# Kernel tuning notes

Hardware: AMD Instinct MI355X
Metric: run time of the kernel (lower is better)

Reference implementation:

```python
import jax, jax.numpy as jnp
import numpy as np

B, N, E, D = 1, 50000, 800000, 128


def _mlp(x, w1, b1, w2, b2, w3, b3):
    # MLP(in, hidden, out, l=2): Linear+ReLU, Linear+ReLU, Linear
    h = jax.nn.relu(x @ w1 + b1)
    h = jax.nn.relu(h @ w2 + b2)
    return h @ w3 + b3


def _glorot(key, shape):
    fan_in, fan_out = shape[0], shape[1]
    lim = np.sqrt(6.0 / (fan_in + fan_out)).astype(np.float32)
    return jax.random.uniform(key, shape, jnp.float32, -lim, lim)


def setup_inputs() -> dict:
    key = jax.random.key(0)
    ks = jax.random.split(key, 16)
    inp = {
        "nodes": jax.random.normal(ks[0], (B, N, D), jnp.float32),
        "senders": jax.random.randint(ks[1], (E,), 0, N, jnp.int32),
        "receivers": jax.random.randint(ks[2], (E,), 0, N, jnp.int32),
        # message MLP params: 2D -> D -> D -> D
        "mw1": _glorot(ks[3], (2 * D, D)), "mb1": jnp.zeros((D,), jnp.float32),
        "mw2": _glorot(ks[4], (D, D)),     "mb2": jnp.zeros((D,), jnp.float32),
        "mw3": _glorot(ks[5], (D, D)),     "mb3": jnp.zeros((D,), jnp.float32),
        # node MLP params: 2D -> D -> D -> D
        "nw1": _glorot(ks[6], (2 * D, D)), "nb1": jnp.zeros((D,), jnp.float32),
        "nw2": _glorot(ks[7], (D, D)),     "nb2": jnp.zeros((D,), jnp.float32),
        "nw3": _glorot(ks[8], (D, D)),     "nb3": jnp.zeros((D,), jnp.float32),
    }
    return inp


def reference(nodes, senders, receivers,
              mw1, mb1, mw2, mb2, mw3, mb3,
              nw1, nb1, nw2, nb2, nw3, nb3):
    # gather endpoint features: [B, E, 2D]
    edge_in = jnp.concatenate((nodes[:, receivers], nodes[:, senders]), axis=-1)
    messages = _mlp(edge_in, mw1, mb1, mw2, mb2, mw3, mb3)  # [B, E, D]
    # scatter-add messages into receiver inbox: [B, N, D]
    inbox = jnp.zeros_like(nodes).at[:, receivers].add(messages)
    node_in = jnp.concatenate((nodes, inbox), axis=-1)  # [B, N, 2D]
    return nodes + _mlp(node_in, nw1, nb1, nw2, nb2, nw3, nb3)
```

## Files before the change

### kernel.cpp

```cpp
#include <hip/hip_runtime.h>
#include <hip/hip_bf16.h>
#include <stdint.h>

typedef __bf16 bf16;
typedef bf16 bf16x8 __attribute__((ext_vector_type(8)));
typedef float f32x4 __attribute__((ext_vector_type(4)));

#define N_NODES 50000
#define FEAT 128
#define NB_SCAN ((N_NODES + 1023) / 1024)

static constexpr size_t UV_BYTES    = (size_t)N_NODES * 256 * 2;
static constexpr size_t INBOX_BYTES = (size_t)N_NODES * FEAT * 4;

#define WUV_OFF 0
#define WM2_OFF 32768
#define WM3_OFF 49152
#define WN1_OFF 65536
#define WN2_OFF 98304
#define WN3_OFF 114688
#define W_TOTAL 131072
static constexpr size_t W_BYTES = (size_t)W_TOTAL * 2;

__device__ __forceinline__ bf16x8 cvt_f32x8_bf16(const float* __restrict__ p) {
  float4 f0 = *(const float4*)p;
  float4 f1 = *(const float4*)(p + 4);
  bf16x8 t;
  t[0] = (bf16)f0.x; t[1] = (bf16)f0.y; t[2] = (bf16)f0.z; t[3] = (bf16)f0.w;
  t[4] = (bf16)f1.x; t[5] = (bf16)f1.y; t[6] = (bf16)f1.z; t[7] = (bf16)f1.w;
  return t;
}

__global__ void prep_weights_kernel(const float* __restrict__ mw1, const float* __restrict__ mw2,
                                    const float* __restrict__ mw3, const float* __restrict__ nw1,
                                    const float* __restrict__ nw2, const float* __restrict__ nw3,
                                    bf16* __restrict__ w) {
  int i = blockIdx.x * blockDim.x + threadIdx.x;
  if (i >= W_TOTAL) return;
  float v;
  if (i < WM2_OFF) {
    int c = i >> 7, k = i & 127;
    v = (c < 128) ? mw1[k * 128 + c] : mw1[(128 + k) * 128 + (c - 128)];
  } else if (i < WM3_OFF) {
    int j = i - WM2_OFF; int c = j >> 7, k = j & 127;
    v = mw2[k * 128 + c];
  } else if (i < WN1_OFF) {
    int j = i - WM3_OFF; int c = j >> 7, k = j & 127;
    v = mw3[k * 128 + c];
  } else if (i < WN2_OFF) {
    int j = i - WN1_OFF; int c = j >> 8, k = j & 255;
    v = nw1[k * 128 + c];
  } else if (i < WN3_OFF) {
    int j = i - WN2_OFF; int c = j >> 7, k = j & 127;
    v = nw2[k * 128 + c];
  } else {
    int j = i - WN3_OFF; int c = j >> 7, k = j & 127;
    v = nw3[k * 128 + c];
  }
  w[i] = (bf16)v;
}

__global__ void hist_kernel(const int* __restrict__ receivers, int* __restrict__ cnt, int E) {
  int i = blockIdx.x * blockDim.x + threadIdx.x;
  if (i < E) atomicAdd(&cnt[receivers[i]], 1);
}

__global__ __launch_bounds__(1024) void scan1_kernel(const int* __restrict__ cnt,
                                                     int* __restrict__ offs,
                                                     int* __restrict__ bsum) {
  __shared__ int s[1024];
  const int tid = threadIdx.x;
  const int g = blockIdx.x * 1024 + tid;
  int x = (g < N_NODES) ? cnt[g] : 0;
  s[tid] = x;
  __syncthreads();
  for (int off = 1; off < 1024; off <<= 1) {
    int v = (tid >= off) ? s[tid - off] : 0;
    __syncthreads();
    s[tid] += v;
    __syncthreads();
  }
  if (g < N_NODES) offs[g] = s[tid] - x;
  if (tid == 1023) bsum[blockIdx.x] = s[tid];
}

__global__ void scan2_kernel(int* __restrict__ bsum) {
  __shared__ int s[64];
  const int tid = threadIdx.x;
  int x = (tid < NB_SCAN) ? bsum[tid] : 0;
  s[tid] = x;
  __syncthreads();
  for (int off = 1; off < 64; off <<= 1) {
    int v = (tid >= off) ? s[tid - off] : 0;
    __syncthreads();
    s[tid] += v;
    __syncthreads();
  }
  if (tid < NB_SCAN) bsum[tid] = s[tid] - x;
}

__global__ void scatter_ids_kernel(const int* __restrict__ senders,
                                   const int* __restrict__ receivers,
                                   const int* __restrict__ offs, const int* __restrict__ bsum,
                                   int* __restrict__ cur,
                                   int* __restrict__ sSend, int* __restrict__ sRecv, int E) {
  int i = blockIdx.x * blockDim.x + threadIdx.x;
  if (i < E) {
    int r = receivers[i];
    int slot = offs[r] + bsum[r >> 10] + atomicAdd(&cur[r], 1);
    sSend[slot] = senders[i];
    sRecv[slot] = r;
  }
}

__global__ void inbox_init_kernel(const int* __restrict__ cnt, const float* __restrict__ mb3,
                                  float* __restrict__ inbox) {
  int i = blockIdx.x * blockDim.x + threadIdx.x;
  if (i >= N_NODES * 32) return;
  int n = i >> 5, q = i & 31;
  float c = (float)cnt[n];
  float4 b = *(const float4*)(mb3 + q * 4);
  float4 o = {c * b.x, c * b.y, c * b.z, c * b.w};
  *(float4*)(inbox + (size_t)n * FEAT + q * 4) = o;
}

__global__ __launch_bounds__(512) void uv_gemm_kernel(const float* __restrict__ nodes,
                                                      const bf16* __restrict__ wuvt,
                                                      const float* __restrict__ mb1,
                                                      bf16* __restrict__ uv) {
  const int tid = threadIdx.x;
  const int lane = tid & 63, wid = tid >> 6;
  const int wm = wid >> 2, wn = wid & 3;
  const int rBase = blockIdx.x * 128 + wm * 64;
  const int cBase = wn * 64;
  const int l15 = lane & 15, ka = (lane >> 4) * 8, rj = (lane >> 4) * 4;

  f32x4 acc[4][4];
#pragma unroll
  for (int mi = 0; mi < 4; ++mi)
#pragma unroll
    for (int ni = 0; ni < 4; ++ni) acc[mi][ni] = (f32x4){0.f, 0.f, 0.f, 0.f};

#pragma unroll
  for (int kk = 0; kk < 4; ++kk) {
    const int k0 = kk * 32 + ka;
    bf16x8 a[4], b[4];
#pragma unroll
    for (int mi = 0; mi < 4; ++mi) {
      int r = rBase + mi * 16 + l15;
      if (r > N_NODES - 1) r = N_NODES - 1;
      a[mi] = cvt_f32x8_bf16(nodes + (size_t)r * FEAT + k0);
    }
#pragma unroll
    for (int ni = 0; ni < 4; ++ni) {
      int c = cBase + ni * 16 + l15;
      b[ni] = *(const bf16x8*)(wuvt + (size_t)c * 128 + k0);
    }
#pragma unroll
    for (int mi = 0; mi < 4; ++mi)
#pragma unroll
      for (int ni = 0; ni < 4; ++ni)
        acc[mi][ni] = __builtin_amdgcn_mfma_f32_16x16x32_bf16(a[mi], b[ni], acc[mi][ni], 0, 0, 0);
  }
#pragma unroll
  for (int mi = 0; mi < 4; ++mi)
#pragma unroll
    for (int ni = 0; ni < 4; ++ni) {
      int c = cBase + ni * 16 + l15;
      float bias = (c < FEAT) ? mb1[c] : 0.f;
#pragma unroll
      for (int j = 0; j < 4; ++j) {
        int r = rBase + mi * 16 + rj + j;
        if (r < N_NODES) uv[(size_t)r * 256 + c] = (bf16)(acc[mi][ni][j] + bias);
      }
    }
}

__device__ __forceinline__ void seg_reduce(const f32x4 (&acc3)[2][8], int idr,
                                           int lane, int l15, int rj,
                                           float* __restrict__ inbox) {
  int nxt = __shfl(idr, (lane & 31) + 1);
  bool bnd = ((lane & 31) == 31) || (idr != nxt);
  unsigned long long bm = __ballot(bnd);
  uint32_t mask = (uint32_t)(bm & 0xffffffffull);
  int lo = 0;
  while (mask) {
    int hi = __ffs(mask) - 1;
    mask &= mask - 1;
    int recv = __shfl(idr, hi);
    if (recv >= 0) {
      float s[8];
#pragma unroll
      for (int ni = 0; ni < 8; ++ni) {
        float x = 0.f;
#pragma unroll
        for (int mi = 0; mi < 2; ++mi)
#pragma unroll
          for (int j = 0; j < 4; ++j) {
            int row = mi * 16 + rj + j;
            x += (row >= lo && row <= hi) ? acc3[mi][ni][j] : 0.f;
          }
        x += __shfl_xor(x, 16);
        x += __shfl_xor(x, 32);
        s[ni] = x;
      }
      if (lane < 16) {
        float* dst = inbox + (size_t)recv * FEAT + l15;
#pragma unroll
        for (int ni = 0; ni < 8; ++ni) unsafeAtomicAdd(dst + ni * 16, s[ni]);
      }
    }
    lo = hi + 1;
  }
}

__global__ __launch_bounds__(256, 3) void edge_kernel(const bf16* __restrict__ uv,
                                                      const int* __restrict__ sSend,
                                                      const int* __restrict__ sRecv,
                                                      const bf16* __restrict__ wm2t,
                                                      const bf16* __restrict__ wm3t,
                                                      const float* __restrict__ mb2,
                                                      float* __restrict__ inbox, int E) {
  __shared__ bf16 hbuf[4][32 * 128];
  const int tid = threadIdx.x, lane = tid & 63, wid = tid >> 6;
  const int l15 = lane & 15, ka = (lane >> 4) * 8, rj = (lane >> 4) * 4;
  const int l31 = lane & 31;
  bf16* hw = hbuf[wid];

  const int e0 = (blockIdx.x * 4 + wid) * 32;
  if (e0 >= E) return;

  int e = e0 + l31;
  bool val = e < E;
  int ec = val ? e : E - 1;
  int idr = val ? sRecv[ec] : -1;
  int ids = sSend[ec];

  int rid[2], sid[2];
#pragma unroll
  for (int mi = 0; mi < 2; ++mi) {
    int row = mi * 16 + l15;
    int rv = __shfl(idr, row);
    rid[mi] = rv < 0 ? 0 : rv;
    sid[mi] = __shfl(ids, row);
  }
  bf16x8 afr[2][4];
#pragma unroll
  for (int mi = 0; mi < 2; ++mi) {
    const bf16* up = uv + (size_t)rid[mi] * 256;
    const bf16* vp = uv + (size_t)sid[mi] * 256 + 128;
#pragma unroll
    for (int kk = 0; kk < 4; ++kk) {
      bf16x8 u8 = *(const bf16x8*)(up + kk * 32 + ka);
      bf16x8 v8 = *(const bf16x8*)(vp + kk * 32 + ka);
      bf16x8 h;
#pragma unroll
      for (int x = 0; x < 8; ++x) {
        float s = (float)u8[x] + (float)v8[x];
        h[x] = (bf16)(s > 0.f ? s : 0.f);
      }
      afr[mi][kk] = h;
    }
  }

  f32x4 acc[2][8];
#pragma unroll
  for (int mi = 0; mi < 2; ++mi)
#pragma unroll
    for (int ni = 0; ni < 8; ++ni) acc[mi][ni] = (f32x4){0.f, 0.f, 0.f, 0.f};
  __builtin_amdgcn_s_setprio(1);
#pragma unroll
  for (int kk = 0; kk < 4; ++kk) {
    const int k0 = kk * 32 + ka;
    bf16x8 b[8];
#pragma unroll
    for (int ni = 0; ni < 8; ++ni) {
      int c = ni * 16 + l15;
      b[ni] = *(const bf16x8*)(wm2t + (size_t)c * 128 + k0);
    }
#pragma unroll
    for (int mi = 0; mi < 2; ++mi)
#pragma unroll
      for (int ni = 0; ni < 8; ++ni)
        acc[mi][ni] = __builtin_amdgcn_mfma_f32_16x16x32_bf16(afr[mi][kk], b[ni], acc[mi][ni], 0, 0, 0);
  }
  __builtin_amdgcn_s_setprio(0);

#pragma unroll
  for (int mi = 0; mi < 2; ++mi)
#pragma unroll
    for (int ni = 0; ni < 8; ++ni) {
      int c = ni * 16 + l15;
      float bias = mb2[c];
#pragma unroll
      for (int j = 0; j < 4; ++j) {
        int row = mi * 16 + rj + j;
        float v = acc[mi][ni][j] + bias;
        v = v > 0.f ? v : 0.f;
        int byte = row * 256 + ((c * 2) ^ ((row & 7) << 4));
        *(bf16*)((char*)hw + byte) = (bf16)v;
      }
    }
  asm volatile("s_waitcnt lgkmcnt(0)" ::: "memory");
  __builtin_amdgcn_sched_barrier(0);

  bf16x8 a3[2][4];
#pragma unroll
  for (int mi = 0; mi < 2; ++mi) {
    int row = mi * 16 + l15;
#pragma unroll
    for (int kk = 0; kk < 4; ++kk) {
      int k0 = kk * 32 + ka;
      int byte = row * 256 + ((k0 * 2) ^ ((row & 7) << 4));
      a3[mi][kk] = *(const bf16x8*)((const char*)hw + byte);
    }
  }
  f32x4 acc3[2][8];
#pragma unroll
  for (int mi = 0; mi < 2; ++mi)
#pragma unroll
    for (int ni = 0; ni < 8; ++ni) acc3[mi][ni] = (f32x4){0.f, 0.f, 0.f, 0.f};
  __builtin_amdgcn_s_setprio(1);
#pragma unroll
  for (int kk = 0; kk < 4; ++kk) {
    const int k0 = kk * 32 + ka;
    bf16x8 b[8];
#pragma unroll
    for (int ni = 0; ni < 8; ++ni) {
      int c = ni * 16 + l15;
      b[ni] = *(const bf16x8*)(wm3t + (size_t)c * 128 + k0);
    }
#pragma unroll
    for (int mi = 0; mi < 2; ++mi)
#pragma unroll
      for (int ni = 0; ni < 8; ++ni)
        acc3[mi][ni] = __builtin_amdgcn_mfma_f32_16x16x32_bf16(a3[mi][kk], b[ni], acc3[mi][ni], 0, 0, 0);
  }
  __builtin_amdgcn_s_setprio(0);

  seg_reduce(acc3, idr, lane, l15, rj, inbox);
}

__global__ __launch_bounds__(256) void node_kernel(const float* __restrict__ nodes,
                                                   const float* __restrict__ inbox,
                                                   const bf16* __restrict__ wn1t,
                                                   const bf16* __restrict__ wn2t,
                                                   const bf16* __restrict__ wn3t,
                                                   const float* __restrict__ nb1,
                                                   const float* __restrict__ nb2,
                                                   const float* __restrict__ nb3,
                                                   float* __restrict__ out) {
  __shared__ bf16 h[128 * 128];
  const int tid = threadIdx.x;
  const int lane = tid & 63, wid = tid >> 6;
  const int wm = wid >> 1, wn = wid & 1;
  const int rBase = wm * 64, cBase = wn * 64;
  const int l15 = lane & 15, ka = (lane >> 4) * 8, rj = (lane >> 4) * 4;
  const int nBase = blockIdx.x * 128;

  f32x4 acc[4][4];
#pragma unroll
  for (int mi = 0; mi < 4; ++mi)
#pragma unroll
    for (int ni = 0; ni < 4; ++ni) acc[mi][ni] = (f32x4){0.f, 0.f, 0.f, 0.f};
#pragma unroll
  for (int kk = 0; kk < 8; ++kk) {
    const int k0 = kk * 32 + ka;
    bf16x8 a[4], b[4];
#pragma unroll
    for (int mi = 0; mi < 4; ++mi) {
      int n = nBase + rBase + mi * 16 + l15;
      if (n > N_NODES - 1) n = N_NODES - 1;
      const float* src = (kk < 4) ? (nodes + (size_t)n * FEAT + k0)
                                  : (inbox + (size_t)n * FEAT + (k0 - 128));
      a[mi] = cvt_f32x8_bf16(src);
    }
#pragma unroll
    for (int ni = 0; ni < 4; ++ni) {
      int c = cBase + ni * 16 + l15;
      b[ni] = *(const bf16x8*)(wn1t + (size_t)c * 256 + k0);
    }
#pragma unroll
    for (int mi = 0; mi < 4; ++mi)
#pragma unroll
      for (int ni = 0; ni < 4; ++ni)
        acc[mi][ni] = __builtin_amdgcn_mfma_f32_16x16x32_bf16(a[mi], b[ni], acc[mi][ni], 0, 0, 0);
  }
#pragma unroll
  for (int mi = 0; mi < 4; ++mi)
#pragma unroll
    for (int ni = 0; ni < 4; ++ni) {
      int c = cBase + ni * 16 + l15;
      float bias = nb1[c];
#pragma unroll
      for (int j = 0; j < 4; ++j) {
        int r = rBase + mi * 16 + rj + j;
        float v = acc[mi][ni][j] + bias;
        v = v > 0.f ? v : 0.f;
        int byte = r * 256 + ((c * 2) ^ ((r & 7) << 4));
        *(bf16*)((char*)h + byte) = (bf16)v;
      }
    }
  __syncthreads();

#pragma unroll
  for (int mi = 0; mi < 4; ++mi)
#pragma unroll
    for (int ni = 0; ni < 4; ++ni) acc[mi][ni] = (f32x4){0.f, 0.f, 0.f, 0.f};
#pragma unroll
  for (int kk = 0; kk < 4; ++kk) {
    const int k0 = kk * 32 + ka;
    bf16x8 a[4], b[4];
#pragma unroll
    for (int mi = 0; mi < 4; ++mi) {
      int r = rBase + mi * 16 + l15;
      int byte = r * 256 + ((k0 * 2) ^ ((r & 7) << 4));
      a[mi] = *(const bf16x8*)((const char*)h + byte);
    }
#pragma unroll
    for (int ni = 0; ni < 4; ++ni) {
      int c = cBase + ni * 16 + l15;
      b[ni] = *(const bf16x8*)(wn2t + (size_t)c * 128 + k0);
    }
#pragma unroll
    for (int mi = 0; mi < 4; ++mi)
#pragma unroll
      for (int ni = 0; ni < 4; ++ni)
        acc[mi][ni] = __builtin_amdgcn_mfma_f32_16x16x32_bf16(a[mi], b[ni], acc[mi][ni], 0, 0, 0);
  }
  __syncthreads();
#pragma unroll
  for (int mi = 0; mi < 4; ++mi)
#pragma unroll
    for (int ni = 0; ni < 4; ++ni) {
      int c = cBase + ni * 16 + l15;
      float bias = nb2[c];
#pragma unroll
      for (int j = 0; j < 4; ++j) {
        int r = rBase + mi * 16 + rj + j;
        float v = acc[mi][ni][j] + bias;
        v = v > 0.f ? v : 0.f;
        int byte = r * 256 + ((c * 2) ^ ((r & 7) << 4));
        *(bf16*)((char*)h + byte) = (bf16)v;
      }
    }
  __syncthreads();

#pragma unroll
  for (int mi = 0; mi < 4; ++mi)
#pragma unroll
    for (int ni = 0; ni < 4; ++ni) acc[mi][ni] = (f32x4){0.f, 0.f, 0.f, 0.f};
#pragma unroll
  for (int kk = 0; kk < 4; ++kk) {
    const int k0 = kk * 32 + ka;
    bf16x8 a[4], b[4];
#pragma unroll
    for (int mi = 0; mi < 4; ++mi) {
      int r = rBase + mi * 16 + l15;
      int byte = r * 256 + ((k0 * 2) ^ ((r & 7) << 4));
      a[mi] = *(const bf16x8*)((const char*)h + byte);
    }
#pragma unroll
    for (int ni = 0; ni < 4; ++ni) {
      int c = cBase + ni * 16 + l15;
      b[ni] = *(const bf16x8*)(wn3t + (size_t)c * 128 + k0);
    }
#pragma unroll
    for (int mi = 0; mi < 4; ++mi)
#pragma unroll
      for (int ni = 0; ni < 4; ++ni)
        acc[mi][ni] = __builtin_amdgcn_mfma_f32_16x16x32_bf16(a[mi], b[ni], acc[mi][ni], 0, 0, 0);
  }
#pragma unroll
  for (int mi = 0; mi < 4; ++mi)
#pragma unroll
    for (int ni = 0; ni < 4; ++ni) {
      int c = cBase + ni * 16 + l15;
      float bias = nb3[c];
#pragma unroll
      for (int j = 0; j < 4; ++j) {
        int r = rBase + mi * 16 + rj + j;
        int n = nBase + r;
        if (n < N_NODES)
          out[(size_t)n * FEAT + c] = nodes[(size_t)n * FEAT + c] + acc[mi][ni][j] + bias;
      }
    }
}

extern "C" void kernel_launch(void* const* d_in, const int* in_sizes, int n_in,
                              void* d_out, int out_size, void* d_ws, size_t ws_size,
                              hipStream_t stream) {
  const float* nodes = (const float*)d_in[0];
  const int* senders = (const int*)d_in[1];
  const int* receivers = (const int*)d_in[2];
  const float* mw1 = (const float*)d_in[3];
  const float* mb1 = (const float*)d_in[4];
  const float* mw2 = (const float*)d_in[5];
  const float* mb2 = (const float*)d_in[6];
  const float* mw3 = (const float*)d_in[7];
  const float* mb3 = (const float*)d_in[8];
  const float* nw1 = (const float*)d_in[9];
  const float* nb1 = (const float*)d_in[10];
  const float* nw2 = (const float*)d_in[11];
  const float* nb2 = (const float*)d_in[12];
  const float* nw3 = (const float*)d_in[13];
  const float* nb3 = (const float*)d_in[14];
  float* out = (float*)d_out;
  const int E = in_sizes[1];

  char* ws = (char*)d_ws;
  bf16* uv = (bf16*)ws;
  bf16* w = (bf16*)(ws + UV_BYTES);
  char* p = ws + UV_BYTES + W_BYTES;
  float* inbox = (float*)p; p += INBOX_BYTES;
  int* offs = (int*)p; p += ((size_t)(N_NODES + 1) * 4 + 255) & ~255ull;
  int* cnt = (int*)p;  p += ((size_t)N_NODES * 4 + 255) & ~255ull;
  int* cur = (int*)p;  p += ((size_t)N_NODES * 4 + 255) & ~255ull;
  int* bsum = (int*)p; p += 256;
  int* sSend = (int*)p; p += ((size_t)E * 4 + 255) & ~255ull;
  int* sRecv = (int*)p; p += ((size_t)E * 4 + 255) & ~255ull;

  hipMemsetAsync(cnt, 0, (size_t)N_NODES * 4, stream);
  hipMemsetAsync(cur, 0, (size_t)N_NODES * 4, stream);
  prep_weights_kernel<<<(W_TOTAL + 255) / 256, 256, 0, stream>>>(mw1, mw2, mw3, nw1, nw2, nw3, w);
  hist_kernel<<<(E + 255) / 256, 256, 0, stream>>>(receivers, cnt, E);
  scan1_kernel<<<NB_SCAN, 1024, 0, stream>>>(cnt, offs, bsum);
  scan2_kernel<<<1, 64, 0, stream>>>(bsum);
  scatter_ids_kernel<<<(E + 255) / 256, 256, 0, stream>>>(senders, receivers, offs, bsum, cur,
                                                          sSend, sRecv, E);
  inbox_init_kernel<<<(N_NODES * 32 + 255) / 256, 256, 0, stream>>>(cnt, mb3, inbox);
  uv_gemm_kernel<<<(N_NODES + 127) / 128, 512, 0, stream>>>(nodes, w + WUV_OFF, mb1, uv);
  edge_kernel<<<(E + 127) / 128, 256, 0, stream>>>(uv, sSend, sRecv, w + WM2_OFF, w + WM3_OFF,
                                                   mb2, inbox, E);
  node_kernel<<<(N_NODES + 127) / 128, 256, 0, stream>>>(nodes, inbox, w + WN1_OFF, w + WN2_OFF,
                                                         w + WN3_OFF, nb1, nb2, nb3, out);
}
```

Baseline: 424.3 us.

## Shrink edge tile to 16 rows per wave and merge prep kernels

Each wave in the edge kernel now handles 16 edges instead of 32. This halves the accumulator registers and LDS per wave and drops the launch_bounds occupancy hint, at the cost of loading the weight fragments twice as often per edge and doing more segmented atomic reductions. Separately, prep_weights and hist are merged into one launch, and scatter_ids and inbox_init are merged into another, to cut kernel-launch overhead.

```diff
diff --git a/kernel.cpp b/kernel.cpp
--- a/kernel.cpp
+++ b/kernel.cpp
@@ -21,6 +21,7 @@
 #define WN3_OFF 114688
 #define W_TOTAL 131072
 static constexpr size_t W_BYTES = (size_t)W_TOTAL * 2;
+#define PREP_BLOCKS ((W_TOTAL + 255) / 256)
 
 __device__ __forceinline__ bf16x8 cvt_f32x8_bf16(const float* __restrict__ p) {
   float4 f0 = *(const float4*)p;
@@ -31,38 +32,40 @@
   return t;
 }
 
-__global__ void prep_weights_kernel(const float* __restrict__ mw1, const float* __restrict__ mw2,
-                                    const float* __restrict__ mw3, const float* __restrict__ nw1,
-                                    const float* __restrict__ nw2, const float* __restrict__ nw3,
-                                    bf16* __restrict__ w) {
-  int i = blockIdx.x * blockDim.x + threadIdx.x;
-  if (i >= W_TOTAL) return;
-  float v;
-  if (i < WM2_OFF) {
-    int c = i >> 7, k = i & 127;
-    v = (c < 128) ? mw1[k * 128 + c] : mw1[(128 + k) * 128 + (c - 128)];
-  } else if (i < WM3_OFF) {
-    int j = i - WM2_OFF; int c = j >> 7, k = j & 127;
-    v = mw2[k * 128 + c];
-  } else if (i < WN1_OFF) {
-    int j = i - WM3_OFF; int c = j >> 7, k = j & 127;
-    v = mw3[k * 128 + c];
-  } else if (i < WN2_OFF) {
-    int j = i - WN1_OFF; int c = j >> 8, k = j & 255;
-    v = nw1[k * 128 + c];
-  } else if (i < WN3_OFF) {
-    int j = i - WN2_OFF; int c = j >> 7, k = j & 127;
-    v = nw2[k * 128 + c];
+__global__ void prep_hist_kernel(const float* __restrict__ mw1, const float* __restrict__ mw2,
+                                 const float* __restrict__ mw3, const float* __restrict__ nw1,
+                                 const float* __restrict__ nw2, const float* __restrict__ nw3,
+                                 bf16* __restrict__ w,
+                                 const int* __restrict__ receivers, int* __restrict__ cnt, int E) {
+  const int b = blockIdx.x;
+  if (b < PREP_BLOCKS) {
+    int i = b * 256 + threadIdx.x;
+    if (i >= W_TOTAL) return;
+    float v;
+    if (i < WM2_OFF) {
+      int c = i >> 7, k = i & 127;
+      v = (c < 128) ? mw1[k * 128 + c] : mw1[(128 + k) * 128 + (c - 128)];
+    } else if (i < WM3_OFF) {
+      int j = i - WM2_OFF; int c = j >> 7, k = j & 127;
+      v = mw2[k * 128 + c];
+    } else if (i < WN1_OFF) {
+      int j = i - WM3_OFF; int c = j >> 7, k = j & 127;
+      v = mw3[k * 128 + c];
+    } else if (i < WN2_OFF) {
+      int j = i - WN1_OFF; int c = j >> 8, k = j & 255;
+      v = nw1[k * 128 + c];
+    } else if (i < WN3_OFF) {
+      int j = i - WN2_OFF; int c = j >> 7, k = j & 127;
+      v = nw2[k * 128 + c];
+    } else {
+      int j = i - WN3_OFF; int c = j >> 7, k = j & 127;
+      v = nw3[k * 128 + c];
+    }
+    w[i] = (bf16)v;
   } else {
-    int j = i - WN3_OFF; int c = j >> 7, k = j & 127;
-    v = nw3[k * 128 + c];
-  }
-  w[i] = (bf16)v;
-}
-
-__global__ void hist_kernel(const int* __restrict__ receivers, int* __restrict__ cnt, int E) {
-  int i = blockIdx.x * blockDim.x + threadIdx.x;
-  if (i < E) atomicAdd(&cnt[receivers[i]], 1);
+    int i = (b - PREP_BLOCKS) * 256 + threadIdx.x;
+    if (i < E) atomicAdd(&cnt[receivers[i]], 1);
+  }
 }
 
 __global__ __launch_bounds__(1024) void scan1_kernel(const int* __restrict__ cnt,
@@ -99,29 +102,32 @@
   if (tid < NB_SCAN) bsum[tid] = s[tid] - x;
 }
 
-__global__ void scatter_ids_kernel(const int* __restrict__ senders,
-                                   const int* __restrict__ receivers,
-                                   const int* __restrict__ offs, const int* __restrict__ bsum,
-                                   int* __restrict__ cur,
-                                   int* __restrict__ sSend, int* __restrict__ sRecv, int E) {
-  int i = blockIdx.x * blockDim.x + threadIdx.x;
-  if (i < E) {
-    int r = receivers[i];
-    int slot = offs[r] + bsum[r >> 10] + atomicAdd(&cur[r], 1);
-    sSend[slot] = senders[i];
-    sRecv[slot] = r;
-  }
-}
-
-__global__ void inbox_init_kernel(const int* __restrict__ cnt, const float* __restrict__ mb3,
-                                  float* __restrict__ inbox) {
-  int i = blockIdx.x * blockDim.x + threadIdx.x;
-  if (i >= N_NODES * 32) return;
-  int n = i >> 5, q = i & 31;
-  float c = (float)cnt[n];
-  float4 b = *(const float4*)(mb3 + q * 4);
-  float4 o = {c * b.x, c * b.y, c * b.z, c * b.w};
-  *(float4*)(inbox + (size_t)n * FEAT + q * 4) = o;
+__global__ void scatter_inbox_kernel(const int* __restrict__ senders,
+                                     const int* __restrict__ receivers,
+                                     const int* __restrict__ offs, const int* __restrict__ bsum,
+                                     int* __restrict__ cur,
+                                     int* __restrict__ sSend, int* __restrict__ sRecv,
+                                     const int* __restrict__ cnt, const float* __restrict__ mb3,
+                                     float* __restrict__ inbox, int E) {
+  const int SC = (E + 255) >> 8;
+  const int b = blockIdx.x;
+  if (b < SC) {
+    int i = b * 256 + threadIdx.x;
+    if (i < E) {
+      int r = receivers[i];
+      int slot = offs[r] + bsum[r >> 10] + atomicAdd(&cur[r], 1);
+      sSend[slot] = senders[i];
+      sRecv[slot] = r;
+    }
+  } else {
+    int i = (b - SC) * 256 + threadIdx.x;
+    if (i >= N_NODES * 32) return;
+    int n = i >> 5, q = i & 31;
+    float c = (float)cnt[n];
+    float4 bb = *(const float4*)(mb3 + q * 4);
+    float4 o = {c * bb.x, c * bb.y, c * bb.z, c * bb.w};
+    *(float4*)(inbox + (size_t)n * FEAT + q * 4) = o;
+  }
 }
 
 __global__ __launch_bounds__(512) void uv_gemm_kernel(const float* __restrict__ nodes,
@@ -176,13 +182,108 @@
     }
 }
 
-__device__ __forceinline__ void seg_reduce(const f32x4 (&acc3)[2][8], int idr,
-                                           int lane, int l15, int rj,
-                                           float* __restrict__ inbox) {
-  int nxt = __shfl(idr, (lane & 31) + 1);
-  bool bnd = ((lane & 31) == 31) || (idr != nxt);
-  unsigned long long bm = __ballot(bnd);
-  uint32_t mask = (uint32_t)(bm & 0xffffffffull);
+__global__ __launch_bounds__(256) void edge_kernel(const bf16* __restrict__ uv,
+                                                   const int* __restrict__ sSend,
+                                                   const int* __restrict__ sRecv,
+                                                   const bf16* __restrict__ wm2t,
+                                                   const bf16* __restrict__ wm3t,
+                                                   const float* __restrict__ mb2,
+                                                   float* __restrict__ inbox, int E) {
+  __shared__ bf16 hbuf[4][16 * 128];
+  const int tid = threadIdx.x, lane = tid & 63, wid = tid >> 6;
+  const int l15 = lane & 15, ka = (lane >> 4) * 8, rj = (lane >> 4) * 4;
+  bf16* hw = hbuf[wid];
+
+  const int e0 = (blockIdx.x * 4 + wid) * 16;
+  if (e0 >= E) return;
+
+  int e = e0 + l15;
+  bool val = e < E;
+  int ec = val ? e : E - 1;
+  int idr = val ? sRecv[ec] : -1;
+  int ids = sSend[ec];
+
+  int rid = idr < 0 ? 0 : idr;
+  const bf16* up = uv + (size_t)rid * 256;
+  const bf16* vp = uv + (size_t)ids * 256 + 128;
+  bf16x8 afr[4];
+#pragma unroll
+  for (int kk = 0; kk < 4; ++kk) {
+    bf16x8 u8 = *(const bf16x8*)(up + kk * 32 + ka);
+    bf16x8 v8 = *(const bf16x8*)(vp + kk * 32 + ka);
+    bf16x8 h;
+#pragma unroll
+    for (int x = 0; x < 8; ++x) {
+      float s = (float)u8[x] + (float)v8[x];
+      h[x] = (bf16)(s > 0.f ? s : 0.f);
+    }
+    afr[kk] = h;
+  }
+
+  f32x4 acc[8];
+#pragma unroll
+  for (int ni = 0; ni < 8; ++ni) acc[ni] = (f32x4){0.f, 0.f, 0.f, 0.f};
+  __builtin_amdgcn_s_setprio(1);
+#pragma unroll
+  for (int kk = 0; kk < 4; ++kk) {
+    const int k0 = kk * 32 + ka;
+    bf16x8 b[8];
+#pragma unroll
+    for (int ni = 0; ni < 8; ++ni) {
+      int c = ni * 16 + l15;
+      b[ni] = *(const bf16x8*)(wm2t + (size_t)c * 128 + k0);
+    }
+#pragma unroll
+    for (int ni = 0; ni < 8; ++ni)
+      acc[ni] = __builtin_amdgcn_mfma_f32_16x16x32_bf16(afr[kk], b[ni], acc[ni], 0, 0, 0);
+  }
+  __builtin_amdgcn_s_setprio(0);
+
+#pragma unroll
+  for (int ni = 0; ni < 8; ++ni) {
+    int c = ni * 16 + l15;
+    float bias = mb2[c];
+#pragma unroll
+    for (int j = 0; j < 4; ++j) {
+      int row = rj + j;
+      float v = acc[ni][j] + bias;
+      v = v > 0.f ? v : 0.f;
+      int byte = row * 256 + ((c * 2) ^ ((row & 7) << 4));
+      *(bf16*)((char*)hw + byte) = (bf16)v;
+    }
+  }
+  asm volatile("s_waitcnt lgkmcnt(0)" ::: "memory");
+  __builtin_amdgcn_sched_barrier(0);
+
+  bf16x8 a3[4];
+#pragma unroll
+  for (int kk = 0; kk < 4; ++kk) {
+    int k0 = kk * 32 + ka;
+    int byte = l15 * 256 + ((k0 * 2) ^ ((l15 & 7) << 4));
+    a3[kk] = *(const bf16x8*)((const char*)hw + byte);
+  }
+  f32x4 acc3[8];
+#pragma unroll
+  for (int ni = 0; ni < 8; ++ni) acc3[ni] = (f32x4){0.f, 0.f, 0.f, 0.f};
+  __builtin_amdgcn_s_setprio(1);
+#pragma unroll
+  for (int kk = 0; kk < 4; ++kk) {
+    const int k0 = kk * 32 + ka;
+    bf16x8 b[8];
+#pragma unroll
+    for (int ni = 0; ni < 8; ++ni) {
+      int c = ni * 16 + l15;
+      b[ni] = *(const bf16x8*)(wm3t + (size_t)c * 128 + k0);
+    }
+#pragma unroll
+    for (int ni = 0; ni < 8; ++ni)
+      acc3[ni] = __builtin_amdgcn_mfma_f32_16x16x32_bf16(a3[kk], b[ni], acc3[ni], 0, 0, 0);
+  }
+  __builtin_amdgcn_s_setprio(0);
+
+  int nxt = __shfl(idr, l15 + 1);
+  bool bnd = (l15 == 15) || (idr != nxt);
+  uint32_t mask = (uint32_t)(__ballot(bnd) & 0xffffull);
   int lo = 0;
   while (mask) {
     int hi = __ffs(mask) - 1;
@@ -194,12 +295,10 @@
       for (int ni = 0; ni < 8; ++ni) {
         float x = 0.f;
 #pragma unroll
-        for (int mi = 0; mi < 2; ++mi)
-#pragma unroll
-          for (int j = 0; j < 4; ++j) {
-            int row = mi * 16 + rj + j;
-            x += (row >= lo && row <= hi) ? acc3[mi][ni][j] : 0.f;
-          }
+        for (int j = 0; j < 4; ++j) {
+          int row = rj + j;
+          x += (row >= lo && row <= hi) ? acc3[ni][j] : 0.f;
+        }
         x += __shfl_xor(x, 16);
         x += __shfl_xor(x, 32);
         s[ni] = x;
@@ -212,133 +311,6 @@
     }
     lo = hi + 1;
   }
-}
-
-__global__ __launch_bounds__(256, 3) void edge_kernel(const bf16* __restrict__ uv,
-                                                      const int* __restrict__ sSend,
-                                                      const int* __restrict__ sRecv,
-                                                      const bf16* __restrict__ wm2t,
-                                                      const bf16* __restrict__ wm3t,
-                                                      const float* __restrict__ mb2,
-                                                      float* __restrict__ inbox, int E) {
-  __shared__ bf16 hbuf[4][32 * 128];
-  const int tid = threadIdx.x, lane = tid & 63, wid = tid >> 6;
-  const int l15 = lane & 15, ka = (lane >> 4) * 8, rj = (lane >> 4) * 4;
-  const int l31 = lane & 31;
-  bf16* hw = hbuf[wid];
-
-  const int e0 = (blockIdx.x * 4 + wid) * 32;
-  if (e0 >= E) return;
-
-  int e = e0 + l31;
-  bool val = e < E;
-  int ec = val ? e : E - 1;
-  int idr = val ? sRecv[ec] : -1;
-  int ids = sSend[ec];
-
-  int rid[2], sid[2];
-#pragma unroll
-  for (int mi = 0; mi < 2; ++mi) {
-    int row = mi * 16 + l15;
-    int rv = __shfl(idr, row);
-    rid[mi] = rv < 0 ? 0 : rv;
-    sid[mi] = __shfl(ids, row);
-  }
-  bf16x8 afr[2][4];
-#pragma unroll
-  for (int mi = 0; mi < 2; ++mi) {
-    const bf16* up = uv + (size_t)rid[mi] * 256;
-    const bf16* vp = uv + (size_t)sid[mi] * 256 + 128;
-#pragma unroll
-    for (int kk = 0; kk < 4; ++kk) {
-      bf16x8 u8 = *(const bf16x8*)(up + kk * 32 + ka);
-      bf16x8 v8 = *(const bf16x8*)(vp + kk * 32 + ka);
-      bf16x8 h;
-#pragma unroll
-      for (int x = 0; x < 8; ++x) {
-        float s = (float)u8[x] + (float)v8[x];
-        h[x] = (bf16)(s > 0.f ? s : 0.f);
-      }
-      afr[mi][kk] = h;
-    }
-  }
-
-  f32x4 acc[2][8];
-#pragma unroll
-  for (int mi = 0; mi < 2; ++mi)
-#pragma unroll
-    for (int ni = 0; ni < 8; ++ni) acc[mi][ni] = (f32x4){0.f, 0.f, 0.f, 0.f};
-  __builtin_amdgcn_s_setprio(1);
-#pragma unroll
-  for (int kk = 0; kk < 4; ++kk) {
-    const int k0 = kk * 32 + ka;
-    bf16x8 b[8];
-#pragma unroll
-    for (int ni = 0; ni < 8; ++ni) {
-      int c = ni * 16 + l15;
-      b[ni] = *(const bf16x8*)(wm2t + (size_t)c * 128 + k0);
-    }
-#pragma unroll
-    for (int mi = 0; mi < 2; ++mi)
-#pragma unroll
-      for (int ni = 0; ni < 8; ++ni)
-        acc[mi][ni] = __builtin_amdgcn_mfma_f32_16x16x32_bf16(afr[mi][kk], b[ni], acc[mi][ni], 0, 0, 0);
-  }
-  __builtin_amdgcn_s_setprio(0);
-
-#pragma unroll
-  for (int mi = 0; mi < 2; ++mi)
-#pragma unroll
-    for (int ni = 0; ni < 8; ++ni) {
-      int c = ni * 16 + l15;
-      float bias = mb2[c];
-#pragma unroll
-      for (int j = 0; j < 4; ++j) {
-        int row = mi * 16 + rj + j;
-        float v = acc[mi][ni][j] + bias;
-        v = v > 0.f ? v : 0.f;
-        int byte = row * 256 + ((c * 2) ^ ((row & 7) << 4));
-        *(bf16*)((char*)hw + byte) = (bf16)v;
-      }
-    }
-  asm volatile("s_waitcnt lgkmcnt(0)" ::: "memory");
-  __builtin_amdgcn_sched_barrier(0);
-
-  bf16x8 a3[2][4];
-#pragma unroll
-  for (int mi = 0; mi < 2; ++mi) {
-    int row = mi * 16 + l15;
-#pragma unroll
-    for (int kk = 0; kk < 4; ++kk) {
-      int k0 = kk * 32 + ka;
-      int byte = row * 256 + ((k0 * 2) ^ ((row & 7) << 4));
-      a3[mi][kk] = *(const bf16x8*)((const char*)hw + byte);
-    }
-  }
-  f32x4 acc3[2][8];
-#pragma unroll
-  for (int mi = 0; mi < 2; ++mi)
-#pragma unroll
-    for (int ni = 0; ni < 8; ++ni) acc3[mi][ni] = (f32x4){0.f, 0.f, 0.f, 0.f};
-  __builtin_amdgcn_s_setprio(1);
-#pragma unroll
-  for (int kk = 0; kk < 4; ++kk) {
-    const int k0 = kk * 32 + ka;
-    bf16x8 b[8];
-#pragma unroll
-    for (int ni = 0; ni < 8; ++ni) {
-      int c = ni * 16 + l15;
-      b[ni] = *(const bf16x8*)(wm3t + (size_t)c * 128 + k0);
-    }
-#pragma unroll
-    for (int mi = 0; mi < 2; ++mi)
-#pragma unroll
-      for (int ni = 0; ni < 8; ++ni)
-        acc3[mi][ni] = __builtin_amdgcn_mfma_f32_16x16x32_bf16(a3[mi][kk], b[ni], acc3[mi][ni], 0, 0, 0);
-  }
-  __builtin_amdgcn_s_setprio(0);
-
-  seg_reduce(acc3, idr, lane, l15, rj, inbox);
 }
 
 __global__ __launch_bounds__(256) void node_kernel(const float* __restrict__ nodes,
@@ -520,18 +492,20 @@
   int* sSend = (int*)p; p += ((size_t)E * 4 + 255) & ~255ull;
   int* sRecv = (int*)p; p += ((size_t)E * 4 + 255) & ~255ull;
 
+  const int SC = (E + 255) / 256;
+  const int IB = (N_NODES * 32 + 255) / 256;
+
   hipMemsetAsync(cnt, 0, (size_t)N_NODES * 4, stream);
   hipMemsetAsync(cur, 0, (size_t)N_NODES * 4, stream);
-  prep_weights_kernel<<<(W_TOTAL + 255) / 256, 256, 0, stream>>>(mw1, mw2, mw3, nw1, nw2, nw3, w);
-  hist_kernel<<<(E + 255) / 256, 256, 0, stream>>>(receivers, cnt, E);
+  prep_hist_kernel<<<PREP_BLOCKS + SC, 256, 0, stream>>>(mw1, mw2, mw3, nw1, nw2, nw3, w,
+                                                         receivers, cnt, E);
   scan1_kernel<<<NB_SCAN, 1024, 0, stream>>>(cnt, offs, bsum);
   scan2_kernel<<<1, 64, 0, stream>>>(bsum);
-  scatter_ids_kernel<<<(E + 255) / 256, 256, 0, stream>>>(senders, receivers, offs, bsum, cur,
-                                                          sSend, sRecv, E);
-  inbox_init_kernel<<<(N_NODES * 32 + 255) / 256, 256, 0, stream>>>(cnt, mb3, inbox);
+  scatter_inbox_kernel<<<SC + IB, 256, 0, stream>>>(senders, receivers, offs, bsum, cur,
+                                                    sSend, sRecv, cnt, mb3, inbox, E);
   uv_gemm_kernel<<<(N_NODES + 127) / 128, 512, 0, stream>>>(nodes, w + WUV_OFF, mb1, uv);
-  edge_kernel<<<(E + 127) / 128, 256, 0, stream>>>(uv, sSend, sRecv, w + WM2_OFF, w + WM3_OFF,
-                                                   mb2, inbox, E);
+  edge_kernel<<<(E + 63) / 64, 256, 0, stream>>>(uv, sSend, sRecv, w + WM2_OFF, w + WM3_OFF,
+                                                 mb2, inbox, E);
   node_kernel<<<(N_NODES + 127) / 128, 256, 0, stream>>>(nodes, inbox, w + WN1_OFF, w + WN2_OFF,
                                                          w + WN3_OFF, nb1, nb2, nb3, out);
 }
```

New measurement: 580.5 us. 36.8% more time.
